# Kernel optimization log

Measured on AMD Instinct MI355X. Metric: run time of the kernel, lower is better.

The kernel has to match this reference:

```python
import jax, jax.numpy as jnp
import numpy as np

# Module hyperparameters (init_kwargs): dim=128, res=128, idx=0, split_size=8, num_heads=8
B, RES, DIM, NH = 8, 128, 128, 8
HD = DIM // NH               # head_dim = 16
HSP, WSP = RES, 8            # idx=0 -> H_sp=res, W_sp=split_size
N = HSP * WSP                # tokens per window
SCALE = HD ** -0.5
L = RES * RES


def setup_inputs() -> dict:
    key = jax.random.key(0)
    k1, k2, k3 = jax.random.split(key, 3)
    return {
        "qkv": jax.random.normal(k1, (3, B, L, DIM), dtype=jnp.float32),
        "conv_w": jax.random.normal(k2, (DIM, 1, 3, 3), dtype=jnp.float32) * 0.1,
        "conv_b": jax.random.normal(k3, (DIM,), dtype=jnp.float32) * 0.1,
    }


def _im2cswin(x):
    # x: [B, L, C] -> windows as heads: [B*nW, NH, N, HD]
    x = jnp.transpose(x, (0, 2, 1)).reshape(B, DIM, RES, RES)
    x = x.reshape(B, DIM, RES // HSP, HSP, RES // WSP, WSP)
    x = jnp.transpose(x, (0, 2, 4, 3, 5, 1)).reshape(-1, N, DIM)
    x = x.reshape(-1, N, NH, HD)
    return jnp.transpose(x, (0, 2, 1, 3))


def reference(qkv, conv_w, conv_b):
    q, k, v = qkv[0], qkv[1], qkv[2]
    k = _im2cswin(k)                               # [W, NH, N, HD]
    v = _im2cswin(v)                               # [W, NH, N, HD]

    # q -> per-window image blocks [B*nW, C, H_sp, W_sp]
    qi = jnp.transpose(q, (0, 2, 1)).reshape(B, DIM, RES, RES)
    qi = qi.reshape(B, DIM, RES // HSP, HSP, RES // WSP, WSP)
    qi = jnp.transpose(qi, (0, 2, 4, 1, 3, 5)).reshape(-1, DIM, HSP, WSP)

    # depthwise 3x3 conv LePE
    lepe = jax.lax.conv_general_dilated(
        qi, conv_w, window_strides=(1, 1), padding='SAME',
        feature_group_count=DIM,
        dimension_numbers=('NCHW', 'OIHW', 'NCHW'))
    lepe = lepe + conv_b[None, :, None, None]
    lepe = jnp.transpose(lepe.reshape(-1, NH, HD, N), (0, 1, 3, 2))  # [W, NH, N, HD]
    qh = jnp.transpose(qi.reshape(-1, NH, HD, N), (0, 1, 3, 2))      # [W, NH, N, HD]

    # linear attention: softmax over scaled K^T V (d x d)
    att = jnp.einsum('wnid,wnie->wnde', k, v) * SCALE                # [W, NH, HD, HD]
    att = jax.nn.softmax(att, axis=-1)
    x = jnp.einsum('wnid,wnde->wnie', qh, att) + lepe                # [W, NH, N, HD]

    # windows -> image -> [B, L, C]
    x = jnp.transpose(x, (0, 2, 1, 3)).reshape(-1, N, DIM)
    x = x.reshape(B, RES // HSP, RES // WSP, HSP, WSP, DIM)
    x = jnp.transpose(x, (0, 1, 3, 2, 4, 5)).reshape(B, RES, RES, DIM)
    return x.reshape(B, L, DIM)
```

## Files before the change

### kernel.cpp

```cpp
#include <hip/hip_runtime.h>


static constexpr int BB   = 8;
static constexpr int RES  = 128;
static constexpr int DIM  = 128;
static constexpr int WSP  = 8;
static constexpr int L    = RES * RES;
static constexpr int NWIN = BB * (RES / WSP);
static constexpr float SCALE = 0.25f;
static constexpr int S1 = 4;
static constexpr int S2 = 8;

#define GLD_LDS16(g, l)                                                        \
  __builtin_amdgcn_global_load_lds(                                            \
      (const __attribute__((address_space(1))) void*)(const void*)(g),         \
      (__attribute__((address_space(3))) void*)(l), 16, 0, 0)

__global__ __launch_bounds__(256, 2) void kt_kv_kernel(
    const float* __restrict__ Kg, const float* __restrict__ Vg,
    float* __restrict__ part) {
  __shared__ float K_lds[2][4 * 1024];
  __shared__ float V_lds[2][4 * 1024];

  const int blk = blockIdx.x;
  const int w = blk / S1, s = blk % S1;
  const int b = w >> 4, wb = w & 15;
  const int t = threadIdx.x;
  const int wave = t >> 6, lane = t & 63;

  const int h_ = t >> 5;
  const int dq = (t >> 3) & 3;
  const int ep = t & 7;
  const int kaddr = h_ * 16 + dq * 4;
  const int vaddr = h_ * 16 + ep * 2;

  const size_t win_base = (size_t)(b * L + wb * WSP) * DIM;

  float a00 = 0.f, a01 = 0.f, a10 = 0.f, a11 = 0.f;
  float a20 = 0.f, a21 = 0.f, a30 = 0.f, a31 = 0.f;

  auto stage = [&](int tile, int buf) {
    const int r0 = s * 32 + tile * 4;
    for (int i = 0; i < 8; ++i) {
      const int idx = wave * 8 + i;
      const int m   = idx >> 4;
      const int rr  = (idx >> 2) & 3;
      const int kk  = idx & 3;
      const float* src = (m ? Vg : Kg) + win_base +
                         (size_t)(r0 + rr) * RES * DIM + kk * 256 + lane * 4;
      float* dst = (m ? &V_lds[buf][0] : &K_lds[buf][0]) + rr * 1024 + kk * 256;
      GLD_LDS16(src, dst);
    }
  };

  stage(0, 0);
  __syncthreads();

  for (int tt = 0; tt < 8; ++tt) {
    const int cur = tt & 1;
    if (tt < 7) stage(tt + 1, cur ^ 1);
    const float* Kb = &K_lds[cur][0];
    const float* Vb = &V_lds[cur][0];
#pragma unroll 4
    for (int n = 0; n < 32; ++n) {
      const float4 k4 = *reinterpret_cast<const float4*>(&Kb[n * 128 + kaddr]);
      const float2 v2 = *reinterpret_cast<const float2*>(&Vb[n * 128 + vaddr]);
      a00 += k4.x * v2.x; a01 += k4.x * v2.y;
      a10 += k4.y * v2.x; a11 += k4.y * v2.y;
      a20 += k4.z * v2.x; a21 += k4.z * v2.y;
      a30 += k4.w * v2.x; a31 += k4.w * v2.y;
    }
    __syncthreads();
  }

  float* p = part + (size_t)blk * 2048 + h_ * 256 + ep * 2;
  *reinterpret_cast<float2*>(&p[(dq * 4 + 0) * 16]) = make_float2(a00, a01);
  *reinterpret_cast<float2*>(&p[(dq * 4 + 1) * 16]) = make_float2(a10, a11);
  *reinterpret_cast<float2*>(&p[(dq * 4 + 2) * 16]) = make_float2(a20, a21);
  *reinterpret_cast<float2*>(&p[(dq * 4 + 3) * 16]) = make_float2(a30, a31);
}

__global__ __launch_bounds__(256, 2) void attn_lepe_kernel(
    const float* __restrict__ Qg, const float* __restrict__ part,
    const float* __restrict__ cw, const float* __restrict__ cb,
    float* __restrict__ outp) {
  __shared__ float q_lds[18 * 1024];
  __shared__ float A_sm[2048];

  const int blk = blockIdx.x;
  const int w = blk / S2, s2 = blk % S2;
  const int b = w >> 4, wb = w & 15;
  const int t = threadIdx.x;
  const int wave = t >> 6, lane = t & 63;
  const size_t win_base = (size_t)(b * L + wb * WSP) * DIM;
  const int r0 = s2 * 16;

  for (int i = 0; i < 18; ++i) {
    const int idx = wave * 18 + i;
    const int hr = idx >> 2, kk = idx & 3;
    const int g = r0 - 1 + hr;
    float* dst = q_lds + hr * 1024 + kk * 256;
    if ((unsigned)g < 128u) {
      const float* src = Qg + win_base + (size_t)g * RES * DIM + kk * 256 +
                         lane * 4;
      GLD_LDS16(src, dst);
    } else {
      *reinterpret_cast<float4*>(dst + lane * 4) =
          make_float4(0.f, 0.f, 0.f, 0.f);
    }
  }

  {
    const float* pw = part + (size_t)w * (S1 * 2048) + t * 8;
    float4 u0, u1;
    {
      const float4 a0 = *reinterpret_cast<const float4*>(pw);
      const float4 b0 = *reinterpret_cast<const float4*>(pw + 2048);
      const float4 c0 = *reinterpret_cast<const float4*>(pw + 4096);
      const float4 d0 = *reinterpret_cast<const float4*>(pw + 6144);
      u0.x = (a0.x + b0.x + c0.x + d0.x) * SCALE;
      u0.y = (a0.y + b0.y + c0.y + d0.y) * SCALE;
      u0.z = (a0.z + b0.z + c0.z + d0.z) * SCALE;
      u0.w = (a0.w + b0.w + c0.w + d0.w) * SCALE;
      const float4 a1 = *reinterpret_cast<const float4*>(pw + 4);
      const float4 b1 = *reinterpret_cast<const float4*>(pw + 2052);
      const float4 c1 = *reinterpret_cast<const float4*>(pw + 4100);
      const float4 d1 = *reinterpret_cast<const float4*>(pw + 6148);
      u1.x = (a1.x + b1.x + c1.x + d1.x) * SCALE;
      u1.y = (a1.y + b1.y + c1.y + d1.y) * SCALE;
      u1.z = (a1.z + b1.z + c1.z + d1.z) * SCALE;
      u1.w = (a1.w + b1.w + c1.w + d1.w) * SCALE;
    }
    float m = fmaxf(fmaxf(fmaxf(u0.x, u0.y), fmaxf(u0.z, u0.w)),
                    fmaxf(fmaxf(u1.x, u1.y), fmaxf(u1.z, u1.w)));
    m = fmaxf(m, __shfl_xor(m, 1));
    u0.x = __expf(u0.x - m); u0.y = __expf(u0.y - m);
    u0.z = __expf(u0.z - m); u0.w = __expf(u0.w - m);
    u1.x = __expf(u1.x - m); u1.y = __expf(u1.y - m);
    u1.z = __expf(u1.z - m); u1.w = __expf(u1.w - m);
    float ssum = u0.x + u0.y + u0.z + u0.w + u1.x + u1.y + u1.z + u1.w;
    ssum += __shfl_xor(ssum, 1);
    const float rinv = 1.0f / ssum;
    u0.x *= rinv; u0.y *= rinv; u0.z *= rinv; u0.w *= rinv;
    u1.x *= rinv; u1.y *= rinv; u1.z *= rinv; u1.w *= rinv;
    *reinterpret_cast<float4*>(&A_sm[t * 8 + 0]) = u0;
    *reinterpret_cast<float4*>(&A_sm[t * 8 + 4]) = u1;
  }
  __syncthreads();

  const int cq = t & 31, tg = t >> 5;
  const int h_ = cq >> 2;
  const int e0 = (cq & 3) * 4;
  const int c0 = cq * 4;
  float4 Acol[16];
#pragma unroll
  for (int d = 0; d < 16; ++d)
    Acol[d] = *reinterpret_cast<const float4*>(&A_sm[h_ * 256 + d * 16 + e0]);
  float4 wgt[9];
#pragma unroll
  for (int tap = 0; tap < 9; ++tap) {
    wgt[tap].x = cw[(c0 + 0) * 9 + tap];
    wgt[tap].y = cw[(c0 + 1) * 9 + tap];
    wgt[tap].z = cw[(c0 + 2) * 9 + tap];
    wgt[tap].w = cw[(c0 + 3) * 9 + tap];
  }
  const float4 bias = *reinterpret_cast<const float4*>(&cb[c0]);

#define ACC(qs, d)                                                             \
  o.x += (qs) * Acol[d].x; o.y += (qs) * Acol[d].y;                            \
  o.z += (qs) * Acol[d].z; o.w += (qs) * Acol[d].w;
#define CONV(cv, tap)                                                          \
  o.x += cv[dy].x * wgt[tap].x; o.y += cv[dy].y * wgt[tap].y;                  \
  o.z += cv[dy].z * wgt[tap].z; o.w += cv[dy].w * wgt[tap].w;

  const float4 zero4 = make_float4(0.f, 0.f, 0.f, 0.f);

  for (int rsel = 0; rsel < 2; ++rsel) {
    const int lr = tg + rsel * 8;
    const float* rbase = q_lds + lr * 1024;
    float4 cL[3], cC[3];
#pragma unroll
    for (int dy = 0; dy < 3; ++dy) {
      cL[dy] = zero4;
      cC[dy] = *reinterpret_cast<const float4*>(&rbase[dy * 1024 + c0]);
    }
#pragma unroll
    for (int wl = 0; wl < 8; ++wl) {
      float4 cR[3];
#pragma unroll
      for (int dy = 0; dy < 3; ++dy)
        cR[dy] = (wl < 7)
                     ? *reinterpret_cast<const float4*>(
                           &rbase[dy * 1024 + (wl + 1) * 128 + c0])
                     : zero4;
      float4 o = bias;
#pragma unroll
      for (int dy = 0; dy < 3; ++dy) {
        CONV(cL, dy * 3 + 0)
        CONV(cC, dy * 3 + 1)
        CONV(cR, dy * 3 + 2)
      }
      const float* qr = &rbase[1024 + wl * 128 + h_ * 16];
      const float4 q0 = *reinterpret_cast<const float4*>(qr + 0);
      const float4 q1 = *reinterpret_cast<const float4*>(qr + 4);
      const float4 q2 = *reinterpret_cast<const float4*>(qr + 8);
      const float4 q3 = *reinterpret_cast<const float4*>(qr + 12);
      ACC(q0.x, 0)  ACC(q0.y, 1)  ACC(q0.z, 2)  ACC(q0.w, 3)
      ACC(q1.x, 4)  ACC(q1.y, 5)  ACC(q1.z, 6)  ACC(q1.w, 7)
      ACC(q2.x, 8)  ACC(q2.y, 9)  ACC(q2.z, 10) ACC(q2.w, 11)
      ACC(q3.x, 12) ACC(q3.y, 13) ACC(q3.z, 14) ACC(q3.w, 15)

      float* dst = outp + win_base + (size_t)(r0 + lr) * RES * DIM +
                   wl * DIM + c0;
      *reinterpret_cast<float4*>(dst) = o;

#pragma unroll
      for (int dy = 0; dy < 3; ++dy) { cL[dy] = cC[dy]; cC[dy] = cR[dy]; }
    }
  }
#undef ACC
#undef CONV
}

extern "C" void kernel_launch(void* const* d_in, const int* in_sizes, int n_in,
                              void* d_out, int out_size, void* d_ws,
                              size_t ws_size, hipStream_t stream) {
  const float* qkv = (const float*)d_in[0];
  const float* cw  = (const float*)d_in[1];
  const float* cb  = (const float*)d_in[2];
  const float* Qg = qkv;
  const float* Kg = qkv + (size_t)BB * L * DIM;
  const float* Vg = Kg + (size_t)BB * L * DIM;
  float* part = (float*)d_ws;
  float* outp = (float*)d_out;

  kt_kv_kernel<<<NWIN * S1, 256, 0, stream>>>(Kg, Vg, part);
  attn_lepe_kernel<<<NWIN * S2, 256, 0, stream>>>(Qg, part, cw, cb, outp);
}
```

Measured before the change: 58.36 us.

## Fuse KV reduction and attention+LePE into one kernel split by channel group

Replaces the two-kernel pipeline (K^T V partial sums to workspace, then softmax+apply+conv) with a single kernel. Each block owns one window and a 32-channel group (two heads), computes the full K^T V over all 128 rows with a cross-wave LDS reduction, then streams Q tiles with double-buffered async loads for the attention product and depthwise conv. This removes the workspace round trip and the second launch. In exchange each block has a long serial loop over 128 rows, loads are narrower (128-byte row segments), and the grid shrinks from 1024 plus 512 blocks to a single 512-block launch.

```diff
diff --git a/kernel.cpp b/kernel.cpp
--- a/kernel.cpp
+++ b/kernel.cpp
@@ -6,65 +6,57 @@
 static constexpr int DIM  = 128;
 static constexpr int WSP  = 8;
 static constexpr int L    = RES * RES;
-static constexpr int NWIN = BB * (RES / WSP);
 static constexpr float SCALE = 0.25f;
-static constexpr int S1 = 4;
-static constexpr int S2 = 8;
 
 #define GLD_LDS16(g, l)                                                        \
   __builtin_amdgcn_global_load_lds(                                            \
       (const __attribute__((address_space(1))) void*)(const void*)(g),         \
       (__attribute__((address_space(3))) void*)(l), 16, 0, 0)
 
-__global__ __launch_bounds__(256, 2) void kt_kv_kernel(
-    const float* __restrict__ Kg, const float* __restrict__ Vg,
-    float* __restrict__ part) {
-  __shared__ float K_lds[2][4 * 1024];
-  __shared__ float V_lds[2][4 * 1024];
-
-  const int blk = blockIdx.x;
-  const int w = blk / S1, s = blk % S1;
-  const int b = w >> 4, wb = w & 15;
-  const int t = threadIdx.x;
+__global__ __launch_bounds__(256, 2) void fused_lepe(
+    const float* __restrict__ Qg, const float* __restrict__ Kg,
+    const float* __restrict__ Vg, const float* __restrict__ cw,
+    const float* __restrict__ cb, float* __restrict__ outp) {
+  __shared__ float smem[16896];
+  float* const A_sm = smem + 16384;
+
+  const int b  = blockIdx.x;
+  const int w  = b >> 2, g = b & 3;
+  const int bi = w >> 4, wb = w & 15;
+  const int t  = threadIdx.x;
   const int wave = t >> 6, lane = t & 63;
-
-  const int h_ = t >> 5;
-  const int dq = (t >> 3) & 3;
-  const int ep = t & 7;
-  const int kaddr = h_ * 16 + dq * 4;
-  const int vaddr = h_ * 16 + ep * 2;
-
-  const size_t win_base = (size_t)(b * L + wb * WSP) * DIM;
-
-  float a00 = 0.f, a01 = 0.f, a10 = 0.f, a11 = 0.f;
-  float a20 = 0.f, a21 = 0.f, a30 = 0.f, a31 = 0.f;
-
-  auto stage = [&](int tile, int buf) {
-    const int r0 = s * 32 + tile * 4;
-    for (int i = 0; i < 8; ++i) {
-      const int idx = wave * 8 + i;
-      const int m   = idx >> 4;
-      const int rr  = (idx >> 2) & 3;
-      const int kk  = idx & 3;
-      const float* src = (m ? Vg : Kg) + win_base +
-                         (size_t)(r0 + rr) * RES * DIM + kk * 256 + lane * 4;
-      float* dst = (m ? &V_lds[buf][0] : &K_lds[buf][0]) + rr * 1024 + kk * 256;
+  const size_t win_base = (size_t)(bi * L + wb * WSP) * DIM;
+  const int ch0 = g * 32;
+
+  const int h1 = lane >> 5, dq = (lane >> 3) & 3, ep = lane & 7;
+  float a00=0.f,a01=0.f,a10=0.f,a11=0.f,a20=0.f,a21=0.f,a30=0.f,a31=0.f;
+
+  auto stageKV = [&](int tile, int buf) {
+    for (int c = wave; c < 32; c += 4) {
+      const int mat = c >> 4, rr = c & 15;
+      const int r = tile * 16 + rr;
+      const float* src = (mat ? Vg : Kg) + win_base +
+                         (size_t)r * (RES * DIM) + (lane >> 3) * DIM + ch0 +
+                         (lane & 7) * 4;
+      float* dst = smem + mat * 8192 + buf * 4096 + rr * 256;
       GLD_LDS16(src, dst);
     }
   };
 
-  stage(0, 0);
+  stageKV(0, 0);
   __syncthreads();
-
   for (int tt = 0; tt < 8; ++tt) {
     const int cur = tt & 1;
-    if (tt < 7) stage(tt + 1, cur ^ 1);
-    const float* Kb = &K_lds[cur][0];
-    const float* Vb = &V_lds[cur][0];
+    if (tt < 7) stageKV(tt + 1, cur ^ 1);
+    const float* Kb = smem + cur * 4096;
+    const float* Vb = smem + 8192 + cur * 4096;
+    const int n0 = wave * 32;
 #pragma unroll 4
-    for (int n = 0; n < 32; ++n) {
-      const float4 k4 = *reinterpret_cast<const float4*>(&Kb[n * 128 + kaddr]);
-      const float2 v2 = *reinterpret_cast<const float2*>(&Vb[n * 128 + vaddr]);
+    for (int n = n0; n < n0 + 32; ++n) {
+      const float4 k4 =
+          *reinterpret_cast<const float4*>(&Kb[n * 32 + h1 * 16 + dq * 4]);
+      const float2 v2 =
+          *reinterpret_cast<const float2*>(&Vb[n * 32 + h1 * 16 + ep * 2]);
       a00 += k4.x * v2.x; a01 += k4.x * v2.y;
       a10 += k4.y * v2.x; a11 += k4.y * v2.y;
       a20 += k4.z * v2.x; a21 += k4.z * v2.y;
@@ -73,134 +65,112 @@
     __syncthreads();
   }
 
-  float* p = part + (size_t)blk * 2048 + h_ * 256 + ep * 2;
-  *reinterpret_cast<float2*>(&p[(dq * 4 + 0) * 16]) = make_float2(a00, a01);
-  *reinterpret_cast<float2*>(&p[(dq * 4 + 1) * 16]) = make_float2(a10, a11);
-  *reinterpret_cast<float2*>(&p[(dq * 4 + 2) * 16]) = make_float2(a20, a21);
-  *reinterpret_cast<float2*>(&p[(dq * 4 + 3) * 16]) = make_float2(a30, a31);
-}
-
-__global__ __launch_bounds__(256, 2) void attn_lepe_kernel(
-    const float* __restrict__ Qg, const float* __restrict__ part,
-    const float* __restrict__ cw, const float* __restrict__ cb,
-    float* __restrict__ outp) {
-  __shared__ float q_lds[18 * 1024];
-  __shared__ float A_sm[2048];
-
-  const int blk = blockIdx.x;
-  const int w = blk / S2, s2 = blk % S2;
-  const int b = w >> 4, wb = w & 15;
-  const int t = threadIdx.x;
-  const int wave = t >> 6, lane = t & 63;
-  const size_t win_base = (size_t)(b * L + wb * WSP) * DIM;
-  const int r0 = s2 * 16;
-
-  for (int i = 0; i < 18; ++i) {
-    const int idx = wave * 18 + i;
-    const int hr = idx >> 2, kk = idx & 3;
-    const int g = r0 - 1 + hr;
-    float* dst = q_lds + hr * 1024 + kk * 256;
-    if ((unsigned)g < 128u) {
-      const float* src = Qg + win_base + (size_t)g * RES * DIM + kk * 256 +
-                         lane * 4;
-      GLD_LDS16(src, dst);
-    } else {
-      *reinterpret_cast<float4*>(dst + lane * 4) =
-          make_float4(0.f, 0.f, 0.f, 0.f);
-    }
-  }
+  auto stageQ = [&](int tile, int buf) {
+    const int r0 = tile * 16;
+    float* qb = smem + buf * 4608;
+    for (int c = wave; c < 18; c += 4) {
+      const int r = r0 - 1 + c;
+      float* dst = qb + c * 256;
+      if ((unsigned)r < 128u) {
+        const float* src = Qg + win_base + (size_t)r * (RES * DIM) +
+                           (lane >> 3) * DIM + ch0 + (lane & 7) * 4;
+        GLD_LDS16(src, dst);
+      } else {
+        *reinterpret_cast<float4*>(dst + lane * 4) =
+            make_float4(0.f, 0.f, 0.f, 0.f);
+      }
+    }
+  };
+
+  stageQ(0, 1);
 
   {
-    const float* pw = part + (size_t)w * (S1 * 2048) + t * 8;
-    float4 u0, u1;
-    {
-      const float4 a0 = *reinterpret_cast<const float4*>(pw);
-      const float4 b0 = *reinterpret_cast<const float4*>(pw + 2048);
-      const float4 c0 = *reinterpret_cast<const float4*>(pw + 4096);
-      const float4 d0 = *reinterpret_cast<const float4*>(pw + 6144);
-      u0.x = (a0.x + b0.x + c0.x + d0.x) * SCALE;
-      u0.y = (a0.y + b0.y + c0.y + d0.y) * SCALE;
-      u0.z = (a0.z + b0.z + c0.z + d0.z) * SCALE;
-      u0.w = (a0.w + b0.w + c0.w + d0.w) * SCALE;
-      const float4 a1 = *reinterpret_cast<const float4*>(pw + 4);
-      const float4 b1 = *reinterpret_cast<const float4*>(pw + 2052);
-      const float4 c1 = *reinterpret_cast<const float4*>(pw + 4100);
-      const float4 d1 = *reinterpret_cast<const float4*>(pw + 6148);
-      u1.x = (a1.x + b1.x + c1.x + d1.x) * SCALE;
-      u1.y = (a1.y + b1.y + c1.y + d1.y) * SCALE;
-      u1.z = (a1.z + b1.z + c1.z + d1.z) * SCALE;
-      u1.w = (a1.w + b1.w + c1.w + d1.w) * SCALE;
-    }
-    float m = fmaxf(fmaxf(fmaxf(u0.x, u0.y), fmaxf(u0.z, u0.w)),
-                    fmaxf(fmaxf(u1.x, u1.y), fmaxf(u1.z, u1.w)));
+    float* sc = smem + wave * 512 + lane * 8;
+    sc[0]=a00; sc[1]=a01; sc[2]=a10; sc[3]=a11;
+    sc[4]=a20; sc[5]=a21; sc[6]=a30; sc[7]=a31;
+  }
+  __syncthreads();
+
+  {
+    const int r  = t >> 3;
+    const int e2 = t & 7;
+    const int h = r >> 4, d = r & 15;
+    const int f = (h * 32 + (d >> 2) * 8 + e2) * 8 + (d & 3) * 2;
+    float v0 = smem[f]     + smem[512 + f]     + smem[1024 + f]     + smem[1536 + f];
+    float v1 = smem[f + 1] + smem[512 + f + 1] + smem[1024 + f + 1] + smem[1536 + f + 1];
+    v0 *= SCALE; v1 *= SCALE;
+    float m = fmaxf(v0, v1);
     m = fmaxf(m, __shfl_xor(m, 1));
-    u0.x = __expf(u0.x - m); u0.y = __expf(u0.y - m);
-    u0.z = __expf(u0.z - m); u0.w = __expf(u0.w - m);
-    u1.x = __expf(u1.x - m); u1.y = __expf(u1.y - m);
-    u1.z = __expf(u1.z - m); u1.w = __expf(u1.w - m);
-    float ssum = u0.x + u0.y + u0.z + u0.w + u1.x + u1.y + u1.z + u1.w;
+    m = fmaxf(m, __shfl_xor(m, 2));
+    m = fmaxf(m, __shfl_xor(m, 4));
+    v0 = __expf(v0 - m); v1 = __expf(v1 - m);
+    float ssum = v0 + v1;
     ssum += __shfl_xor(ssum, 1);
+    ssum += __shfl_xor(ssum, 2);
+    ssum += __shfl_xor(ssum, 4);
     const float rinv = 1.0f / ssum;
-    u0.x *= rinv; u0.y *= rinv; u0.z *= rinv; u0.w *= rinv;
-    u1.x *= rinv; u1.y *= rinv; u1.z *= rinv; u1.w *= rinv;
-    *reinterpret_cast<float4*>(&A_sm[t * 8 + 0]) = u0;
-    *reinterpret_cast<float4*>(&A_sm[t * 8 + 4]) = u1;
+    A_sm[r * 16 + e2 * 2 + 0] = v0 * rinv;
+    A_sm[r * 16 + e2 * 2 + 1] = v1 * rinv;
   }
   __syncthreads();
 
-  const int cq = t & 31, tg = t >> 5;
-  const int h_ = cq >> 2;
-  const int e0 = (cq & 3) * 4;
-  const int c0 = cq * 4;
+  const int cq   = t & 7;
+  const int lr   = (t >> 3) & 15;
+  const int half = t >> 7;
+  const int hg = cq >> 2, e0 = (cq & 3) * 4;
+  const int cg = ch0 + cq * 4;
+
   float4 Acol[16];
 #pragma unroll
   for (int d = 0; d < 16; ++d)
-    Acol[d] = *reinterpret_cast<const float4*>(&A_sm[h_ * 256 + d * 16 + e0]);
+    Acol[d] = *reinterpret_cast<const float4*>(&A_sm[(hg * 16 + d) * 16 + e0]);
   float4 wgt[9];
 #pragma unroll
   for (int tap = 0; tap < 9; ++tap) {
-    wgt[tap].x = cw[(c0 + 0) * 9 + tap];
-    wgt[tap].y = cw[(c0 + 1) * 9 + tap];
-    wgt[tap].z = cw[(c0 + 2) * 9 + tap];
-    wgt[tap].w = cw[(c0 + 3) * 9 + tap];
-  }
-  const float4 bias = *reinterpret_cast<const float4*>(&cb[c0]);
+    wgt[tap].x = cw[(cg + 0) * 9 + tap];
+    wgt[tap].y = cw[(cg + 1) * 9 + tap];
+    wgt[tap].z = cw[(cg + 2) * 9 + tap];
+    wgt[tap].w = cw[(cg + 3) * 9 + tap];
+  }
+  const float4 bias = *reinterpret_cast<const float4*>(&cb[cg]);
 
 #define ACC(qs, d)                                                             \
   o.x += (qs) * Acol[d].x; o.y += (qs) * Acol[d].y;                            \
   o.z += (qs) * Acol[d].z; o.w += (qs) * Acol[d].w;
-#define CONV(cv, tap)                                                          \
-  o.x += cv[dy].x * wgt[tap].x; o.y += cv[dy].y * wgt[tap].y;                  \
-  o.z += cv[dy].z * wgt[tap].z; o.w += cv[dy].w * wgt[tap].w;
-
-  const float4 zero4 = make_float4(0.f, 0.f, 0.f, 0.f);
-
-  for (int rsel = 0; rsel < 2; ++rsel) {
-    const int lr = tg + rsel * 8;
-    const float* rbase = q_lds + lr * 1024;
-    float4 cL[3], cC[3];
-#pragma unroll
-    for (int dy = 0; dy < 3; ++dy) {
-      cL[dy] = zero4;
-      cC[dy] = *reinterpret_cast<const float4*>(&rbase[dy * 1024 + c0]);
-    }
-#pragma unroll
-    for (int wl = 0; wl < 8; ++wl) {
-      float4 cR[3];
+
+  int buf = 1;
+  for (int tile = 0; tile < 8; ++tile) {
+    if (tile < 7) stageQ(tile + 1, buf ^ 1);
+    const float* Qb = smem + buf * 4608;
+    const int r0 = tile * 16;
+    const int w0 = half * 4;
+
+    float4 cL[3], cC[3], cR[3];
+    auto ldcol = [&](int cidx, float4* dstv) {
 #pragma unroll
       for (int dy = 0; dy < 3; ++dy)
-        cR[dy] = (wl < 7)
-                     ? *reinterpret_cast<const float4*>(
-                           &rbase[dy * 1024 + (wl + 1) * 128 + c0])
-                     : zero4;
+        dstv[dy] = ((unsigned)cidx < 8u)
+                       ? *reinterpret_cast<const float4*>(
+                             &Qb[((lr + dy) * 8 + cidx) * 32 + cq * 4])
+                       : make_float4(0.f, 0.f, 0.f, 0.f);
+    };
+    ldcol(w0 - 1, cL);
+    ldcol(w0, cC);
+
+#pragma unroll
+    for (int k = 0; k < 4; ++k) {
+      const int wl = w0 + k;
+      ldcol(wl + 1, cR);
       float4 o = bias;
 #pragma unroll
       for (int dy = 0; dy < 3; ++dy) {
-        CONV(cL, dy * 3 + 0)
-        CONV(cC, dy * 3 + 1)
-        CONV(cR, dy * 3 + 2)
+        const int t0 = dy * 3;
+        o.x += cL[dy].x * wgt[t0].x + cC[dy].x * wgt[t0+1].x + cR[dy].x * wgt[t0+2].x;
+        o.y += cL[dy].y * wgt[t0].y + cC[dy].y * wgt[t0+1].y + cR[dy].y * wgt[t0+2].y;
+        o.z += cL[dy].z * wgt[t0].z + cC[dy].z * wgt[t0+1].z + cR[dy].z * wgt[t0+2].z;
+        o.w += cL[dy].w * wgt[t0].w + cC[dy].w * wgt[t0+1].w + cR[dy].w * wgt[t0+2].w;
       }
-      const float* qr = &rbase[1024 + wl * 128 + h_ * 16];
+      const float* qr = &Qb[((lr + 1) * 8 + wl) * 32 + hg * 16];
       const float4 q0 = *reinterpret_cast<const float4*>(qr + 0);
       const float4 q1 = *reinterpret_cast<const float4*>(qr + 4);
       const float4 q2 = *reinterpret_cast<const float4*>(qr + 8);
@@ -210,16 +180,17 @@
       ACC(q2.x, 8)  ACC(q2.y, 9)  ACC(q2.z, 10) ACC(q2.w, 11)
       ACC(q3.x, 12) ACC(q3.y, 13) ACC(q3.z, 14) ACC(q3.w, 15)
 
-      float* dst = outp + win_base + (size_t)(r0 + lr) * RES * DIM +
-                   wl * DIM + c0;
+      float* dst = outp + win_base + (size_t)(r0 + lr) * (RES * DIM) +
+                   wl * DIM + cg;
       *reinterpret_cast<float4*>(dst) = o;
 
 #pragma unroll
       for (int dy = 0; dy < 3; ++dy) { cL[dy] = cC[dy]; cC[dy] = cR[dy]; }
     }
+    __syncthreads();
+    buf ^= 1;
   }
 #undef ACC
-#undef CONV
 }
 
 extern "C" void kernel_launch(void* const* d_in, const int* in_sizes, int n_in,
@@ -231,9 +202,7 @@
   const float* Qg = qkv;
   const float* Kg = qkv + (size_t)BB * L * DIM;
   const float* Vg = Kg + (size_t)BB * L * DIM;
-  float* part = (float*)d_ws;
   float* outp = (float*)d_out;
 
-  kt_kv_kernel<<<NWIN * S1, 256, 0, stream>>>(Kg, Vg, part);
-  attn_lepe_kernel<<<NWIN * S2, 256, 0, stream>>>(Qg, part, cw, cb, outp);
+  fused_lepe<<<512, 256, 0, stream>>>(Qg, Kg, Vg, cw, cb, outp);
 }
```

Result: faster. 55.29 us (-5.3%).
